# Performance work log

Hardware: AMD Instinct MI355X
Metric: run time of the kernel (lower is better)

The kernel has to match this reference:

```python
import jax, jax.numpy as jnp
import numpy as np

E = 8      # num_experts
D = 1024   # input_size
H = 2048   # expert hidden
O = 1024   # output_size
N = 8192   # tokens


def setup_inputs() -> dict:
    key = jax.random.key(0)
    ks = jax.random.split(key, 7)
    s_in = 1.0 / np.sqrt(D)
    s_h = 1.0 / np.sqrt(H)
    return {
        "x": jax.random.normal(ks[0], (N, D), dtype=jnp.float32),
        "Wr": jax.random.normal(ks[1], (D, E), dtype=jnp.float32) * s_in,
        "br": jnp.zeros((E,), dtype=jnp.float32),
        "W1": jax.random.normal(ks[2], (E, D, H), dtype=jnp.float32) * s_in,
        "b1": jnp.zeros((E, H), dtype=jnp.float32),
        "W2": jax.random.normal(ks[3], (E, H, O), dtype=jnp.float32) * s_h,
        "b2": jnp.zeros((E, O), dtype=jnp.float32),
    }


def _moe(x, Wr, br, W1, b1, W2, b2):
    # Supervised top-1 router: softmax probs, argmax route.
    router_probs = jax.nn.softmax(x @ Wr + br, axis=-1)          # [N, E]
    p_max = jnp.max(router_probs, axis=-1)                       # [N]
    routes = jnp.argmax(router_probs, axis=-1)                   # [N] int
    one_hot = jax.nn.one_hot(routes, E, dtype=x.dtype)           # [N, E]
    counts = one_hot.sum(axis=0)                                 # [E]

    # Per-expert 2-layer MLP on all tokens (vectorized over experts),
    # then select the routed expert's output per token. This is the
    # dense-equivalent of the torch gather/per-expert-forward/scatter.
    h = jax.nn.relu(jnp.einsum("nd,edh->enh", x, W1) + b1[:, None, :])   # [E, N, H]
    ys = jnp.einsum("enh,eho->eno", h, W2) + b2[:, None, :]              # [E, N, O]
    out = jnp.einsum("ne,eno->no", one_hot, ys)                          # [N, O]

    # Straight-through scaling: p_max / sg(p_max) == 1 in fwd, routes grad to router.
    ratio = p_max / jax.lax.stop_gradient(p_max)
    out = out * ratio[:, None]
    return out, router_probs, counts


def reference(x, Wr, br, W1, b1, W2, b2):
    return _moe(x, Wr, br, W1, b1, W2, b2)
```

## Files before the change

### kernel.cpp

```cpp
#include <hip/hip_runtime.h>
#include <hip/hip_bf16.h>

#define NTOK 8192
#define DIN  1024
#define HID  2048
#define OUTD 1024
#define NEXP 8
#define BM 128
#define MAXT (NTOK / BM + NEXP)

typedef short short8 __attribute__((ext_vector_type(8)));
typedef float f32x4 __attribute__((ext_vector_type(4)));

static __device__ __forceinline__ unsigned short f2bf(float f) {
  union { __hip_bfloat16 b; unsigned short u; } cv;
  cv.b = __float2bfloat16(f);
  return cv.u;
}

static __device__ __forceinline__ void gload_lds16(const void* g, void* l) {
  __builtin_amdgcn_global_load_lds(
      (const __attribute__((address_space(1))) void*)g,
      (__attribute__((address_space(3))) void*)l, 16, 0, 0);
}

#define T1BLK 4096
#define T2BLK 4096

static __device__ void transpose_body(const float* __restrict__ W,
                                      unsigned short* __restrict__ WT,
                                      int R, int C, int bx, int by, int e,
                                      float* smemf) {
  float (*tile)[65] = (float(*)[65])smemf;
  const int c0 = bx * 64, r0 = by * 64;
  const int lr = threadIdx.x >> 4;
  const int fc = threadIdx.x & 15;
  const float* Wp = W + ((size_t)e * R + r0) * C + c0;
#pragma unroll
  for (int i = 0; i < 4; ++i) {
    int r = lr + i * 16;
    float4 v = *(const float4*)(Wp + (size_t)r * C + fc * 4);
    tile[r][fc * 4 + 0] = v.x; tile[r][fc * 4 + 1] = v.y;
    tile[r][fc * 4 + 2] = v.z; tile[r][fc * 4 + 3] = v.w;
  }
  __syncthreads();
  unsigned short* Op = WT + ((size_t)e * C + c0) * R + r0;
  const int cc0 = threadIdx.x >> 3;
  const int rc = threadIdx.x & 7;
#pragma unroll
  for (int i = 0; i < 2; ++i) {
    int cc = cc0 + i * 32;
    short8 o;
#pragma unroll
    for (int j = 0; j < 8; ++j) o[j] = (short)f2bf(tile[rc * 8 + j][cc]);
    *(short8*)(Op + (size_t)cc * R + rc * 8) = o;
  }
}

static __device__ void router_body(const float* __restrict__ x,
                                   const float* __restrict__ Wr,
                                   const float* __restrict__ br,
                                   unsigned short* __restrict__ xb,
                                   float* __restrict__ probs_out,
                                   int* __restrict__ routes,
                                   int blk, float* smemf) {
  float (*WrL)[DIN] = (float(*)[DIN])smemf;
  const int tid = threadIdx.x;
#pragma unroll
  for (int rr = 0; rr < 4; ++rr) {
    int row = tid * 4 + rr;
    float4 w0 = *(const float4*)(Wr + (size_t)row * NEXP);
    float4 w1 = *(const float4*)(Wr + (size_t)row * NEXP + 4);
    WrL[0][row] = w0.x; WrL[1][row] = w0.y; WrL[2][row] = w0.z; WrL[3][row] = w0.w;
    WrL[4][row] = w1.x; WrL[5][row] = w1.y; WrL[6][row] = w1.z; WrL[7][row] = w1.w;
  }
  __syncthreads();

  const int lane = tid & 63;
  const int n = blk * 4 + (tid >> 6);
  const float4* xr = (const float4*)(x + (size_t)n * DIN);
  ushort4* xo = (ushort4*)(xb + (size_t)n * DIN);
  float acc[NEXP];
#pragma unroll
  for (int e = 0; e < NEXP; ++e) acc[e] = 0.f;
#pragma unroll
  for (int j = 0; j < 4; ++j) {
    int idx = j * 64 + lane;
    float4 xv = xr[idx];
    ushort4 o = { f2bf(xv.x), f2bf(xv.y), f2bf(xv.z), f2bf(xv.w) };
    xo[idx] = o;
    int r0 = idx * 4;
#pragma unroll
    for (int e = 0; e < NEXP; ++e) {
      float4 wv = *(const float4*)&WrL[e][r0];
      acc[e] += xv.x * wv.x + xv.y * wv.y + xv.z * wv.z + xv.w * wv.w;
    }
  }
#pragma unroll
  for (int m = 1; m < 64; m <<= 1)
#pragma unroll
    for (int e = 0; e < NEXP; ++e) acc[e] += __shfl_xor(acc[e], m);

  if (lane == 0) {
    float lg[NEXP], p[NEXP];
    float mx = -1e30f;
#pragma unroll
    for (int e = 0; e < NEXP; ++e) { lg[e] = acc[e] + br[e]; mx = fmaxf(mx, lg[e]); }
    float s = 0.f;
#pragma unroll
    for (int e = 0; e < NEXP; ++e) { p[e] = expf(lg[e] - mx); s += p[e]; }
    float inv = 1.f / s;
    int best = 0; float bp = -1.f;
#pragma unroll
    for (int e = 0; e < NEXP; ++e) {
      p[e] *= inv;
      probs_out[(size_t)n * NEXP + e] = p[e];
      if (p[e] > bp) { bp = p[e]; best = e; }
    }
    routes[n] = best;
  }
}

__global__ __launch_bounds__(256) void prep_kernel(
    const float* __restrict__ W1, unsigned short* __restrict__ w1t,
    const float* __restrict__ W2, unsigned short* __restrict__ w2t,
    const float* __restrict__ x, const float* __restrict__ Wr,
    const float* __restrict__ br, unsigned short* __restrict__ xb,
    float* __restrict__ probs_out, int* __restrict__ routes) {
  __shared__ float smemf[8192];
  const int bid = blockIdx.x;
  if (bid < T1BLK) {
    int e = bid >> 9, rem = bid & 511;
    transpose_body(W1, w1t, DIN, HID, rem & 31, rem >> 5, e, smemf);
  } else if (bid < T1BLK + T2BLK) {
    int b = bid - T1BLK;
    int e = b >> 9, rem = b & 511;
    transpose_body(W2, w2t, HID, OUTD, rem & 15, rem >> 4, e, smemf);
  } else {
    router_body(x, Wr, br, xb, probs_out, routes, bid - T1BLK - T2BLK, smemf);
  }
}

__global__ __launch_bounds__(256) void hist_scan_kernel(
    const int* __restrict__ routes, int* __restrict__ pad_off,
    int2* __restrict__ tile_table, float* __restrict__ counts_out,
    int* __restrict__ cursor, int* __restrict__ sorted) {
  __shared__ int wsum[4][NEXP];
  __shared__ int pstart[NEXP], pend[NEXP];
  const int tid = threadIdx.x;
  const int lane = tid & 63, w = tid >> 6;
  int cnt[NEXP];
#pragma unroll
  for (int e = 0; e < NEXP; ++e) cnt[e] = 0;
#pragma unroll
  for (int j = 0; j < 8; ++j) {
    int4 r4 = ((const int4*)routes)[tid + 256 * j];
    int rr[4] = {r4.x, r4.y, r4.z, r4.w};
#pragma unroll
    for (int i = 0; i < 4; ++i)
#pragma unroll
      for (int e = 0; e < NEXP; ++e) cnt[e] += (rr[i] == e);
  }
#pragma unroll
  for (int m = 1; m < 64; m <<= 1)
#pragma unroll
    for (int e = 0; e < NEXP; ++e) cnt[e] += __shfl_xor(cnt[e], m);
  if (lane == 0)
#pragma unroll
    for (int e = 0; e < NEXP; ++e) wsum[w][e] = cnt[e];
  __syncthreads();
  if (tid == 0) {
    int off = 0, t = 0;
    for (int e = 0; e < NEXP; ++e) {
      int c = wsum[0][e] + wsum[1][e] + wsum[2][e] + wsum[3][e];
      pad_off[e] = off;
      cursor[e] = 0;
      counts_out[e] = (float)c;
      int tiles = (c + BM - 1) / BM;
      pstart[e] = off + c;
      pend[e] = off + tiles * BM;
      for (int i = 0; i < tiles; ++i) { tile_table[t] = make_int2(e, off + i * BM); ++t; }
      off += tiles * BM;
    }
    for (; t < MAXT; ++t) tile_table[t] = make_int2(-1, 0);
  }
  __syncthreads();
#pragma unroll
  for (int e = 0; e < NEXP; ++e)
    for (int i = pstart[e] + tid; i < pend[e]; i += 256) sorted[i] = -1;
}

__global__ void build_kernel(const int* __restrict__ routes,
                             const int* __restrict__ pad_off,
                             int* __restrict__ cursor,
                             int* __restrict__ sorted) {
  const int n = blockIdx.x * 256 + threadIdx.x;
  const int lane = threadIdx.x & 63;
  const int e = routes[n];
#pragma unroll
  for (int ex = 0; ex < NEXP; ++ex) {
    unsigned long long m = __ballot(e == ex);
    if (e == ex) {
      int leader = __ffsll(m) - 1;
      int rank = __popcll(m & ((1ull << lane) - 1ull));
      int b = 0;
      if (rank == 0) b = atomicAdd(&cursor[ex], (int)__popcll(m));
      b = __shfl(b, leader);
      sorted[pad_off[ex] + b + rank] = n;
    }
  }
}

#define PHASE_SYNC() do { \
    __builtin_amdgcn_sched_barrier(0); \
    __builtin_amdgcn_s_barrier(); \
    __builtin_amdgcn_sched_barrier(0); \
    asm volatile("s_waitcnt lgkmcnt(0)" ::: "memory"); \
    __builtin_amdgcn_sched_barrier(0); } while (0)
#define VM4()  asm volatile("s_waitcnt vmcnt(4)" ::: "memory")
#define VM0()  asm volatile("s_waitcnt vmcnt(0)" ::: "memory")

#define LDA(MH, D) \
  _Pragma("unroll") for (int i_ = 0; i_ < 2; ++i_) \
  _Pragma("unroll") for (int k_ = 0; k_ < 2; ++k_) \
    fa[MH][i_][k_] = *(const short8*)&lds[(D) + (MH) * 4096 + aoff[i_][k_]];
#define LDB(NH, D) \
  _Pragma("unroll") for (int j_ = 0; j_ < 2; ++j_) \
  _Pragma("unroll") for (int k_ = 0; k_ < 2; ++k_) \
    fb[j_][k_] = *(const short8*)&lds[(D) + 8192 + (NH) * 4096 + boff[j_][k_]];
#define MFMA_QUAD(MH, NH) do { __builtin_amdgcn_s_setprio(1); \
  _Pragma("unroll") for (int i_ = 0; i_ < 2; ++i_) \
  _Pragma("unroll") for (int j_ = 0; j_ < 2; ++j_) \
  _Pragma("unroll") for (int k_ = 0; k_ < 2; ++k_) \
    acc[(MH) * 2 + i_][(NH) * 2 + j_] = __builtin_amdgcn_mfma_f32_16x16x32_bf16( \
        fa[MH][i_][k_], fb[j_][k_], acc[(MH) * 2 + i_][(NH) * 2 + j_], 0, 0, 0); \
  __builtin_amdgcn_s_setprio(0); } while (0)

template <int KDIM, int MODE, int NB>
__global__ __launch_bounds__(256, 2) void gemm_moe(
    const unsigned short* __restrict__ A, const unsigned short* __restrict__ WT,
    const float* __restrict__ bias, const int* __restrict__ sorted,
    const int2* __restrict__ tile_table, void* __restrict__ Cout, int NDIM) {
  __shared__ short lds[32768];

  const int nwg = NB * MAXT;
  const int bid = blockIdx.x;
  const int swz = (bid & 7) * (nwg >> 3) + (bid >> 3);
  const int2 tt = tile_table[swz / NB];
  if (tt.x < 0) return;
  const int expert = tt.x, mbase = tt.y;
  const int n0 = (swz % NB) * 128;
  const int tid = threadIdx.x, lane = tid & 63, w = tid >> 6;
  const int qm = w >> 1, qn = w & 1;
  const int fr = lane & 15, klo = lane >> 4;

  const short* srcA[2][2];
  const short* srcB[2][2];
  int dstoff[2];
#pragma unroll
  for (int l = 0; l < 2; ++l) {
    const int ch = l * 256 + tid;
    const int row = ch >> 3;
    const int csw = ((ch & 7) ^ (row & 7)) * 8;
    dstoff[l] = ch * 8;
#pragma unroll
    for (int h = 0; h < 2; ++h) {
      int tok = sorted[mbase + h * 64 + row];
      if (tok < 0) tok = 0;
      srcA[h][l] = (const short*)A + (size_t)tok * KDIM + csw;
      srcB[h][l] = (const short*)WT + ((size_t)expert * NDIM + n0 + h * 64 + row) * KDIM + csw;
    }
  }
  auto stA = [&](int doff, int h, int kt) {
    const int base = doff + h * 4096, ko = kt * 64;
#pragma unroll
    for (int l = 0; l < 2; ++l) gload_lds16(srcA[h][l] + ko, &lds[base + dstoff[l]]);
  };
  auto stB = [&](int doff, int h, int kt) {
    const int base = doff + 8192 + h * 4096, ko = kt * 64;
#pragma unroll
    for (int l = 0; l < 2; ++l) gload_lds16(srcB[h][l] + ko, &lds[base + dstoff[l]]);
  };

  const int rsw = (fr & 7) << 4;
  int aoff[2][2], boff[2][2];
#pragma unroll
  for (int i = 0; i < 2; ++i)
#pragma unroll
    for (int k = 0; k < 2; ++k) {
      int b = (qm * 32 + i * 16 + fr) * 128 + k * 64 + klo * 16;
      aoff[i][k] = (b ^ rsw) >> 1;
    }
#pragma unroll
  for (int j = 0; j < 2; ++j)
#pragma unroll
    for (int k = 0; k < 2; ++k) {
      int b = (qn * 32 + j * 16 + fr) * 128 + k * 64 + klo * 16;
      boff[j][k] = (b ^ rsw) >> 1;
    }

  f32x4 acc[4][4];
#pragma unroll
  for (int mi = 0; mi < 4; ++mi)
#pragma unroll
    for (int nj = 0; nj < 4; ++nj) acc[mi][nj] = (f32x4){0.f, 0.f, 0.f, 0.f};
  short8 fa[2][2][2], fb[2][2];

  constexpr int NKT = KDIM / 64;
  stB(0, 0, 0); stA(0, 1, 0); stB(0, 1, 0); stA(0, 0, 0);
  stB(16384, 0, 1); stA(16384, 1, 1);
  VM4();
  __builtin_amdgcn_s_barrier();
  __builtin_amdgcn_sched_barrier(0);

  for (int t = 0; t < NKT; ++t) {
    const int d = (t & 1) * 16384;
    const int dn = 16384 - d;
    LDA(0, d); LDB(0, d);
    if (t + 1 < NKT) stB(dn, 1, t + 1);
    PHASE_SYNC();
    MFMA_QUAD(0, 0);
    LDA(1, d);
    if (t + 1 < NKT) stA(dn, 0, t + 1);
    PHASE_SYNC();
    MFMA_QUAD(1, 0);
    LDB(1, d);
    if (t + 2 < NKT) stB(d, 0, t + 2);
    PHASE_SYNC();
    MFMA_QUAD(1, 1);
    if (t + 2 < NKT) { stA(d, 1, t + 2); VM4(); } else { VM0(); }
    PHASE_SYNC();
    MFMA_QUAD(0, 1);
  }

  const int fq = lane >> 4;
#pragma unroll
  for (int mi = 0; mi < 4; ++mi) {
    const int rbase = mbase + (mi >> 1) * 64 + qm * 32 + (mi & 1) * 16 + fq * 4;
    int tok[4];
#pragma unroll
    for (int r = 0; r < 4; ++r) tok[r] = sorted[rbase + r];
#pragma unroll
    for (int nj = 0; nj < 4; ++nj) {
      const int col = n0 + (nj >> 1) * 64 + qn * 32 + (nj & 1) * 16 + fr;
      const float bv = bias[(size_t)expert * NDIM + col];
#pragma unroll
      for (int r = 0; r < 4; ++r) {
        if (tok[r] < 0) continue;
        float v = acc[mi][nj][r] + bv;
        if (MODE == 0) {
          ((unsigned short*)Cout)[(size_t)tok[r] * NDIM + col] = f2bf(fmaxf(v, 0.f));
        } else {
          ((float*)Cout)[(size_t)tok[r] * NDIM + col] = v;
        }
      }
    }
  }
}

extern "C" void kernel_launch(void* const* d_in, const int* in_sizes, int n_in,
                              void* d_out, int out_size, void* d_ws, size_t ws_size,
                              hipStream_t stream) {
  const float* x  = (const float*)d_in[0];
  const float* Wr = (const float*)d_in[1];
  const float* br = (const float*)d_in[2];
  const float* W1 = (const float*)d_in[3];
  const float* b1 = (const float*)d_in[4];
  const float* W2 = (const float*)d_in[5];
  const float* b2 = (const float*)d_in[6];

  float* out_y      = (float*)d_out;
  float* out_probs  = out_y + (size_t)NTOK * OUTD;
  float* out_counts = out_probs + (size_t)NTOK * NEXP;

  char* ws = (char*)d_ws;
  unsigned short* xb   = (unsigned short*)(ws);
  unsigned short* w1t  = (unsigned short*)(ws + 16777216ULL);
  unsigned short* w2t  = (unsigned short*)(ws + 50331648ULL);
  unsigned short* hbuf = (unsigned short*)(ws + 83886080ULL);
  char* p = ws + 117440512ULL;
  int* routes   = (int*)p; p += 32768;
  int* sorted   = (int*)p; p += (NTOK + NEXP * BM) * 4;
  int* cursor   = (int*)p; p += 256;
  int* pad_off  = (int*)p; p += 256;
  int2* tt      = (int2*)p;

  prep_kernel<<<T1BLK + T2BLK + NTOK / 4, 256, 0, stream>>>(
      W1, w1t, W2, w2t, x, Wr, br, xb, out_probs, routes);
  hist_scan_kernel<<<1, 256, 0, stream>>>(routes, pad_off, tt, out_counts,
                                          cursor, sorted);
  build_kernel<<<NTOK / 256, 256, 0, stream>>>(routes, pad_off, cursor, sorted);
  gemm_moe<DIN, 0, HID / 128><<<(HID / 128) * MAXT, 256, 0, stream>>>(
      xb, w1t, b1, sorted, tt, hbuf, HID);
  gemm_moe<HID, 1, OUTD / 128><<<(OUTD / 128) * MAXT, 256, 0, stream>>>(
      hbuf, w2t, b2, sorted, tt, out_y, OUTD);
}
```

Before: 189.7 us.

## Overlap W2 transpose with first expert GEMM and vectorize router weight staging

The W2 fp32-to-bf16 transpose blocks move out of the prep kernel and are appended to the first GEMM launch, so the transpose's memory traffic can run alongside the compute-bound GEMM1 tiles instead of sitting in front of hist/scan. The GEMM is refactored into a device body shared by both launches. Router Wr staging into LDS now uses float4 transposed stores instead of scalar writes. The risk is that transpose blocks scheduled after the GEMM blocks only fill the tail, and the combined kernel keeps the GEMM's launch bounds and LDS footprint for the transpose blocks.

```diff
diff --git a/kernel.cpp b/kernel.cpp
--- a/kernel.cpp
+++ b/kernel.cpp
@@ -9,6 +9,11 @@
 #define BM 128
 #define MAXT (NTOK / BM + NEXP)
 
+#define T1BLK 4096
+#define RTBLK (NTOK / 4)
+#define T2BLK 4096
+#define G1BLK ((HID / 128) * MAXT)
+
 typedef short short8 __attribute__((ext_vector_type(8)));
 typedef float f32x4 __attribute__((ext_vector_type(4)));
 
@@ -23,9 +28,6 @@
       (const __attribute__((address_space(1))) void*)g,
       (__attribute__((address_space(3))) void*)l, 16, 0, 0);
 }
-
-#define T1BLK 4096
-#define T2BLK 4096
 
 static __device__ void transpose_body(const float* __restrict__ W,
                                       unsigned short* __restrict__ WT,
@@ -66,13 +68,23 @@
                                    int blk, float* smemf) {
   float (*WrL)[DIN] = (float(*)[DIN])smemf;
   const int tid = threadIdx.x;
-#pragma unroll
-  for (int rr = 0; rr < 4; ++rr) {
-    int row = tid * 4 + rr;
-    float4 w0 = *(const float4*)(Wr + (size_t)row * NEXP);
-    float4 w1 = *(const float4*)(Wr + (size_t)row * NEXP + 4);
-    WrL[0][row] = w0.x; WrL[1][row] = w0.y; WrL[2][row] = w0.z; WrL[3][row] = w0.w;
-    WrL[4][row] = w1.x; WrL[5][row] = w1.y; WrL[6][row] = w1.z; WrL[7][row] = w1.w;
+  {
+    const int r0 = tid * 4;
+    float wlo[4][4], whi[4][4];
+#pragma unroll
+    for (int rr = 0; rr < 4; ++rr) {
+      float4 v0 = *(const float4*)(Wr + (size_t)(r0 + rr) * NEXP);
+      float4 v1 = *(const float4*)(Wr + (size_t)(r0 + rr) * NEXP + 4);
+      wlo[rr][0] = v0.x; wlo[rr][1] = v0.y; wlo[rr][2] = v0.z; wlo[rr][3] = v0.w;
+      whi[rr][0] = v1.x; whi[rr][1] = v1.y; whi[rr][2] = v1.z; whi[rr][3] = v1.w;
+    }
+#pragma unroll
+    for (int e = 0; e < 4; ++e) {
+      float4 o = { wlo[0][e], wlo[1][e], wlo[2][e], wlo[3][e] };
+      *(float4*)&WrL[e][r0] = o;
+      float4 o2 = { whi[0][e], whi[1][e], whi[2][e], whi[3][e] };
+      *(float4*)&WrL[e + 4][r0] = o2;
+    }
   }
   __syncthreads();
 
@@ -121,9 +133,8 @@
   }
 }
 
-__global__ __launch_bounds__(256) void prep_kernel(
+__global__ __launch_bounds__(256) void prep1_kernel(
     const float* __restrict__ W1, unsigned short* __restrict__ w1t,
-    const float* __restrict__ W2, unsigned short* __restrict__ w2t,
     const float* __restrict__ x, const float* __restrict__ Wr,
     const float* __restrict__ br, unsigned short* __restrict__ xb,
     float* __restrict__ probs_out, int* __restrict__ routes) {
@@ -132,12 +143,8 @@
   if (bid < T1BLK) {
     int e = bid >> 9, rem = bid & 511;
     transpose_body(W1, w1t, DIN, HID, rem & 31, rem >> 5, e, smemf);
-  } else if (bid < T1BLK + T2BLK) {
-    int b = bid - T1BLK;
-    int e = b >> 9, rem = b & 511;
-    transpose_body(W2, w2t, HID, OUTD, rem & 15, rem >> 4, e, smemf);
   } else {
-    router_body(x, Wr, br, xb, probs_out, routes, bid - T1BLK - T2BLK, smemf);
+    router_body(x, Wr, br, xb, probs_out, routes, bid - T1BLK, smemf);
   }
 }
 
@@ -237,14 +244,12 @@
   __builtin_amdgcn_s_setprio(0); } while (0)
 
 template <int KDIM, int MODE, int NB>
-__global__ __launch_bounds__(256, 2) void gemm_moe(
+static __device__ void gemm_body(
+    short* lds, int bid,
     const unsigned short* __restrict__ A, const unsigned short* __restrict__ WT,
     const float* __restrict__ bias, const int* __restrict__ sorted,
     const int2* __restrict__ tile_table, void* __restrict__ Cout, int NDIM) {
-  __shared__ short lds[32768];
-
   const int nwg = NB * MAXT;
-  const int bid = blockIdx.x;
   const int swz = (bid & 7) * (nwg >> 3) + (bid >> 3);
   const int2 tt = tile_table[swz / NB];
   if (tt.x < 0) return;
@@ -358,6 +363,33 @@
   }
 }
 
+__global__ __launch_bounds__(256, 2) void gemm1_t2_kernel(
+    const unsigned short* __restrict__ xb, const unsigned short* __restrict__ w1t,
+    const float* __restrict__ b1, const int* __restrict__ sorted,
+    const int2* __restrict__ tile_table, unsigned short* __restrict__ hbuf,
+    const float* __restrict__ W2, unsigned short* __restrict__ w2t) {
+  __shared__ short lds[32768];
+  const int bid = blockIdx.x;
+  if (bid < G1BLK) {
+    gemm_body<DIN, 0, HID / 128>(lds, bid, xb, w1t, b1, sorted, tile_table,
+                                 (void*)hbuf, HID);
+  } else {
+    int b = bid - G1BLK;
+    int e = b >> 9, rem = b & 511;
+    transpose_body(W2, w2t, HID, OUTD, rem & 15, rem >> 4, e, (float*)lds);
+  }
+}
+
+template <int KDIM, int MODE, int NB>
+__global__ __launch_bounds__(256, 2) void gemm_moe(
+    const unsigned short* __restrict__ A, const unsigned short* __restrict__ WT,
+    const float* __restrict__ bias, const int* __restrict__ sorted,
+    const int2* __restrict__ tile_table, void* __restrict__ Cout, int NDIM) {
+  __shared__ short lds[32768];
+  gemm_body<KDIM, MODE, NB>(lds, blockIdx.x, A, WT, bias, sorted, tile_table,
+                            Cout, NDIM);
+}
+
 extern "C" void kernel_launch(void* const* d_in, const int* in_sizes, int n_in,
                               void* d_out, int out_size, void* d_ws, size_t ws_size,
                               hipStream_t stream) {
@@ -385,13 +417,13 @@
   int* pad_off  = (int*)p; p += 256;
   int2* tt      = (int2*)p;
 
-  prep_kernel<<<T1BLK + T2BLK + NTOK / 4, 256, 0, stream>>>(
-      W1, w1t, W2, w2t, x, Wr, br, xb, out_probs, routes);
+  prep1_kernel<<<T1BLK + RTBLK, 256, 0, stream>>>(
+      W1, w1t, x, Wr, br, xb, out_probs, routes);
   hist_scan_kernel<<<1, 256, 0, stream>>>(routes, pad_off, tt, out_counts,
                                           cursor, sorted);
   build_kernel<<<NTOK / 256, 256, 0, stream>>>(routes, pad_off, cursor, sorted);
-  gemm_moe<DIN, 0, HID / 128><<<(HID / 128) * MAXT, 256, 0, stream>>>(
-      xb, w1t, b1, sorted, tt, hbuf, HID);
+  gemm1_t2_kernel<<<G1BLK + T2BLK, 256, 0, stream>>>(
+      xb, w1t, b1, sorted, tt, hbuf, W2, w2t);
   gemm_moe<HID, 1, OUTD / 128><<<(OUTD / 128) * MAXT, 256, 0, stream>>>(
       hbuf, w2t, b2, sorted, tt, out_y, OUTD);
 }
```

Measured after the change: 183.4 us. -3.3%, faster.
